# Optimization experiments

Hardware: AMD Instinct MI355X
Metric: run time of the kernel (lower is better)

## Reference

```python
import jax, jax.numpy as jnp
import numpy as np

EPS = 1e-8
ANGULAR_WEIGHT = 0.1
L2_REG = 1e-4


def gram_schmidt_batch(A):
    # A: (B, 3, 3); orthogonalize the COLUMNS
    u1 = A[:, :, 0]
    e1 = u1 / (jnp.linalg.norm(u1, axis=1, keepdims=True) + EPS)
    a2 = A[:, :, 1]
    u2 = a2 - jnp.sum(e1 * a2, axis=1, keepdims=True) * e1
    e2 = u2 / (jnp.linalg.norm(u2, axis=1, keepdims=True) + EPS)
    a3 = A[:, :, 2]
    u3 = a3 - jnp.sum(e1 * a3, axis=1, keepdims=True) * e1 - jnp.sum(e2 * a3, axis=1, keepdims=True) * e2
    e3 = u3 / (jnp.linalg.norm(u3, axis=1, keepdims=True) + EPS)
    Q = jnp.stack([e1, e2, e3], axis=2)  # (B,3,3), columns e1,e2,e3
    det = jnp.linalg.det(Q)
    # flip third column where det < 0 to ensure proper rotation
    e3_fixed = jnp.where(det[:, None] < 0, -Q[:, :, 2], Q[:, :, 2])
    return Q.at[:, :, 2].set(e3_fixed)


def nine_d_to_rotmat(nine_d):
    A = jnp.clip(nine_d, -10.0, 10.0).reshape(-1, 3, 3)
    return gram_schmidt_batch(A)


def angular_distance(pred_9d, target_9d):
    pred_rot = nine_d_to_rotmat(pred_9d)
    target_rot = nine_d_to_rotmat(target_9d)
    # trace(pred^T @ target) = sum over all entries of elementwise product
    traces = jnp.einsum('bij,bij->b', pred_rot, target_rot)
    traces = jnp.clip(traces, -3.0 + 1e-6, 3.0 - 1e-6)
    cos_angle = jnp.clip((traces - 1.0) / 2.0, -1.0 + 1e-7, 1.0 - 1e-7)
    angles_deg = jnp.arccos(cos_angle) * (180.0 / np.pi)
    return jnp.where(jnp.isnan(angles_deg), 180.0, angles_deg)


def orthogonality_loss(nine_d):
    B = nine_d.shape[0]
    M = nine_d.reshape(B, 3, 3)
    AtA = jnp.einsum('bki,bkj->bij', M, M)
    diff = AtA - jnp.eye(3, dtype=nine_d.dtype)
    return jnp.mean(jnp.sum(diff * diff, axis=(1, 2)))


def setup_inputs() -> dict:
    key = jax.random.key(0)
    k1, k2 = jax.random.split(key)
    B = 4194304
    return {
        'pred_delta_9d': jax.random.normal(k1, (B, 9), dtype=jnp.float32),
        'target_delta_9d': jax.random.normal(k2, (B, 9), dtype=jnp.float32),
    }


def reference(pred_delta_9d, target_delta_9d):
    pred_delta_9d = jnp.clip(pred_delta_9d, -10.0, 10.0)
    pred_rot = nine_d_to_rotmat(pred_delta_9d)
    target_rot = nine_d_to_rotmat(target_delta_9d)
    diff = pred_rot - target_rot
    chordal_loss = jnp.mean(jnp.sum(diff * diff, axis=(1, 2)))
    angular_loss_term = jnp.mean(angular_distance(pred_delta_9d, target_delta_9d))
    ortho_loss = orthogonality_loss(pred_delta_9d)
    l2_loss = jnp.mean(pred_delta_9d ** 2)
    total_loss = chordal_loss + ANGULAR_WEIGHT * angular_loss_term + 0.01 * ortho_loss + L2_REG * l2_loss
    # NaN fallback: MSE between pred and target
    fallback = jnp.mean((pred_delta_9d - target_delta_9d) ** 2)
    return jnp.where(jnp.isnan(total_loss), fallback, total_loss)
```

## Files before the change

kernel.cpp:

```cpp
#include <hip/hip_runtime.h>
#include <math.h>

#define EPS_GS 1e-8f
#define RAD2DEG 57.29577951308232f
#define PI_F 3.14159265358979f
#define NBLOCKS 2048
#define NTHREADS 256

__device__ __forceinline__ float clip10(float x) {
    x = x < -10.f ? -10.f : x;
    x = x >  10.f ?  10.f : x;
    return x;
}

__device__ __forceinline__ float fsqrt(float x) { return __builtin_amdgcn_sqrtf(x); }
__device__ __forceinline__ float frcp(float x)  { return __builtin_amdgcn_rcpf(x); }

__device__ __forceinline__ float fast_acos(float x) {
    float ax = fabsf(x);
    float p = fmaf(ax, -0.0187293f, 0.0742610f);
    p = fmaf(ax, p, -0.2121144f);
    p = fmaf(ax, p, 1.5707288f);
    float pos = fsqrt(1.f - ax) * p;
    return x >= 0.f ? pos : PI_F - pos;
}

__device__ __forceinline__ void gs_rotmat(const float* v, float* R) {
    float c0x = v[0], c0y = v[3], c0z = v[6];
    float c1x = v[1], c1y = v[4], c1z = v[7];
    float c2x = v[2], c2y = v[5], c2z = v[8];

    float s1 = fmaf(c0x, c0x, fmaf(c0y, c0y, c0z*c0z));
    float inv1 = frcp(fsqrt(s1) + EPS_GS);
    float e1x = c0x*inv1, e1y = c0y*inv1, e1z = c0z*inv1;

    float d = fmaf(e1x, c1x, fmaf(e1y, c1y, e1z*c1z));
    float u2x = fmaf(-d, e1x, c1x), u2y = fmaf(-d, e1y, c1y), u2z = fmaf(-d, e1z, c1z);
    float s2 = fmaf(u2x, u2x, fmaf(u2y, u2y, u2z*u2z));
    float inv2 = frcp(fsqrt(s2) + EPS_GS);
    float e2x = u2x*inv2, e2y = u2y*inv2, e2z = u2z*inv2;

    float d1 = fmaf(e1x, c2x, fmaf(e1y, c2y, e1z*c2z));
    float d2 = fmaf(e2x, c2x, fmaf(e2y, c2y, e2z*c2z));
    float u3x = fmaf(-d1, e1x, fmaf(-d2, e2x, c2x));
    float u3y = fmaf(-d1, e1y, fmaf(-d2, e2y, c2y));
    float u3z = fmaf(-d1, e1z, fmaf(-d2, e2z, c2z));
    float s3 = fmaf(u3x, u3x, fmaf(u3y, u3y, u3z*u3z));
    float inv3 = frcp(fsqrt(s3) + EPS_GS);
    float e3x = u3x*inv3, e3y = u3y*inv3, e3z = u3z*inv3;

    float cxx = e2y*e3z - e2z*e3y;
    float cxy = e2z*e3x - e2x*e3z;
    float cxz = e2x*e3y - e2y*e3x;
    float det = fmaf(e1x, cxx, fmaf(e1y, cxy, e1z*cxz));
    if (det < 0.f) { e3x = -e3x; e3y = -e3y; e3z = -e3z; }

    R[0] = e1x; R[1] = e2x; R[2] = e3x;
    R[3] = e1y; R[4] = e2y; R[5] = e3y;
    R[6] = e1z; R[7] = e2z; R[8] = e3z;
}

__device__ __forceinline__ void accum_rot(const float* pr, const float* tg,
                                          float& lt, float& lf) {
    float pc[9], tc[9];
    #pragma unroll
    for (int m = 0; m < 9; ++m) { pc[m] = clip10(pr[m]); tc[m] = clip10(tg[m]); }

    float Rp[9], Rt[9];
    gs_rotmat(pc, Rp);
    gs_rotmat(tc, Rt);

    float chord = 0.f, tr = 0.f;
    #pragma unroll
    for (int m = 0; m < 9; ++m) {
        float d = Rp[m] - Rt[m];
        chord = fmaf(d, d, chord);
        tr    = fmaf(Rp[m], Rt[m], tr);
    }

    const float trLo = -3.0f + 1e-6f, trHi = 3.0f - 1e-6f;
    tr = tr < trLo ? trLo : (tr > trHi ? trHi : tr);
    float ca = (tr - 1.f) * 0.5f;
    const float cLo = -1.0f + 1e-7f, cHi = 1.0f - 1e-7f;
    ca = ca < cLo ? cLo : (ca > cHi ? cHi : ca);
    float ang = fast_acos(ca) * RAD2DEG;
    if (ang != ang) ang = 180.f;

    float o = 0.f;
    #pragma unroll
    for (int i = 0; i < 3; ++i) {
        #pragma unroll
        for (int j = 0; j < 3; ++j) {
            float s = fmaf(pc[i], pc[j], fmaf(pc[3+i], pc[3+j], pc[6+i]*pc[6+j]));
            s -= (i == j) ? 1.f : 0.f;
            o = fmaf(s, s, o);
        }
    }

    float l2 = 0.f, fb = 0.f;
    #pragma unroll
    for (int m = 0; m < 9; ++m) {
        l2 = fmaf(pc[m], pc[m], l2);
        float d = pc[m] - tg[m];
        fb = fmaf(d, d, fb);
    }

    lt += fmaf(0.1f, ang, chord) + fmaf(0.01f, o, (1e-4f/9.f)*l2);
    lf += fb;
}

__global__ __launch_bounds__(NTHREADS)
void rot_loss_kernel(const float* __restrict__ pred, const float* __restrict__ targ,
                     float2* __restrict__ partial, int B) {
    const int ngroups  = (B + 3) >> 2;
    const int nthreads = gridDim.x * blockDim.x;

    float lt = 0.f, lf = 0.f;

    for (int g = blockIdx.x * blockDim.x + threadIdx.x; g < ngroups; g += nthreads) {
        const int base = g * 4;
        if (base + 3 < B) {
            const float4* p4 = reinterpret_cast<const float4*>(pred) + (size_t)g * 9;
            const float4* t4 = reinterpret_cast<const float4*>(targ) + (size_t)g * 9;
            float4 pv[9], tv[9];
            #pragma unroll
            for (int j = 0; j < 9; ++j) pv[j] = p4[j];
            #pragma unroll
            for (int j = 0; j < 9; ++j) tv[j] = t4[j];
            float a[36], b[36];
            #pragma unroll
            for (int j = 0; j < 9; ++j) {
                a[4*j+0] = pv[j].x; a[4*j+1] = pv[j].y; a[4*j+2] = pv[j].z; a[4*j+3] = pv[j].w;
                b[4*j+0] = tv[j].x; b[4*j+1] = tv[j].y; b[4*j+2] = tv[j].z; b[4*j+3] = tv[j].w;
            }
            #pragma unroll
            for (int k = 0; k < 4; ++k) accum_rot(&a[9*k], &b[9*k], lt, lf);
        } else {
            for (int r = base; r < B; ++r) {
                float a1[9], b1[9];
                for (int m = 0; m < 9; ++m) { a1[m] = pred[(size_t)r*9 + m]; b1[m] = targ[(size_t)r*9 + m]; }
                accum_rot(a1, b1, lt, lf);
            }
        }
    }

    #pragma unroll
    for (int off = 32; off > 0; off >>= 1) {
        lt += __shfl_down(lt, off, 64);
        lf += __shfl_down(lf, off, 64);
    }
    __shared__ float st[4], sf[4];
    const int lane = threadIdx.x & 63;
    const int wid  = threadIdx.x >> 6;
    if (lane == 0) { st[wid] = lt; sf[wid] = lf; }
    __syncthreads();
    if (threadIdx.x == 0) {
        float bt = st[0] + st[1] + st[2] + st[3];
        float bf = sf[0] + sf[1] + sf[2] + sf[3];
        partial[blockIdx.x] = make_float2(bt, bf);
    }
}

__global__ __launch_bounds__(256)
void finalize_kernel(const float2* __restrict__ partial, int nparts,
                     float* __restrict__ out, int B) {
    double t = 0.0, f = 0.0;
    for (int i = threadIdx.x; i < nparts; i += 256) {
        float2 p = partial[i];
        t += (double)p.x;
        f += (double)p.y;
    }
    #pragma unroll
    for (int off = 32; off > 0; off >>= 1) {
        t += __shfl_down(t, off, 64);
        f += __shfl_down(f, off, 64);
    }
    __shared__ double st[4], sf[4];
    const int lane = threadIdx.x & 63;
    const int wid  = threadIdx.x >> 6;
    if (lane == 0) { st[wid] = t; sf[wid] = f; }
    __syncthreads();
    if (threadIdx.x == 0) {
        double total = (st[0] + st[1] + st[2] + st[3]) / (double)B;
        double fb    = (sf[0] + sf[1] + sf[2] + sf[3]) / (9.0 * (double)B);
        out[0] = isnan(total) ? (float)fb : (float)total;
    }
}

extern "C" void kernel_launch(void* const* d_in, const int* in_sizes, int n_in,
                              void* d_out, int out_size, void* d_ws, size_t ws_size,
                              hipStream_t stream) {
    const float* pred = (const float*)d_in[0];
    const float* targ = (const float*)d_in[1];
    const int n = in_sizes[0];
    const int B = n / 9;

    float2* partial = (float2*)d_ws;

    rot_loss_kernel<<<NBLOCKS, NTHREADS, 0, stream>>>(pred, targ, partial, B);
    finalize_kernel<<<1, 256, 0, stream>>>(partial, NBLOCKS, (float*)d_out, B);
}
```

Before: 368.6 us.

## Stage rotations through shared memory with coalesced loads, one tile per block

Replaces the grid-stride loop, where each thread loaded 9 strided float4s, with a one-shot kernel. Each block loads 512 rotations of pred and target into LDS using fully coalesced float4 reads, then each thread computes two rotations from LDS. A separate tail kernel handles leftover rows, and the finalize kernel grows to 1024 threads to reduce the larger set of partials (8192 blocks). The cost is 36 KB of LDS per block, which limits occupancy, plus strided 9-float LDS reads per thread that may bank-conflict.

```diff
diff --git a/kernel.cpp b/kernel.cpp
--- a/kernel.cpp
+++ b/kernel.cpp
@@ -4,8 +4,8 @@
 #define EPS_GS 1e-8f
 #define RAD2DEG 57.29577951308232f
 #define PI_F 3.14159265358979f
-#define NBLOCKS 2048
-#define NTHREADS 256
+#define ROT_PER_BLOCK 512
+#define F4_PER_INPUT 1152
 
 __device__ __forceinline__ float clip10(float x) {
     x = x < -10.f ? -10.f : x;
@@ -109,41 +109,7 @@
     lf += fb;
 }
 
-__global__ __launch_bounds__(NTHREADS)
-void rot_loss_kernel(const float* __restrict__ pred, const float* __restrict__ targ,
-                     float2* __restrict__ partial, int B) {
-    const int ngroups  = (B + 3) >> 2;
-    const int nthreads = gridDim.x * blockDim.x;
-
-    float lt = 0.f, lf = 0.f;
-
-    for (int g = blockIdx.x * blockDim.x + threadIdx.x; g < ngroups; g += nthreads) {
-        const int base = g * 4;
-        if (base + 3 < B) {
-            const float4* p4 = reinterpret_cast<const float4*>(pred) + (size_t)g * 9;
-            const float4* t4 = reinterpret_cast<const float4*>(targ) + (size_t)g * 9;
-            float4 pv[9], tv[9];
-            #pragma unroll
-            for (int j = 0; j < 9; ++j) pv[j] = p4[j];
-            #pragma unroll
-            for (int j = 0; j < 9; ++j) tv[j] = t4[j];
-            float a[36], b[36];
-            #pragma unroll
-            for (int j = 0; j < 9; ++j) {
-                a[4*j+0] = pv[j].x; a[4*j+1] = pv[j].y; a[4*j+2] = pv[j].z; a[4*j+3] = pv[j].w;
-                b[4*j+0] = tv[j].x; b[4*j+1] = tv[j].y; b[4*j+2] = tv[j].z; b[4*j+3] = tv[j].w;
-            }
-            #pragma unroll
-            for (int k = 0; k < 4; ++k) accum_rot(&a[9*k], &b[9*k], lt, lf);
-        } else {
-            for (int r = base; r < B; ++r) {
-                float a1[9], b1[9];
-                for (int m = 0; m < 9; ++m) { a1[m] = pred[(size_t)r*9 + m]; b1[m] = targ[(size_t)r*9 + m]; }
-                accum_rot(a1, b1, lt, lf);
-            }
-        }
-    }
-
+__device__ __forceinline__ float2 block_reduce(float lt, float lf) {
     #pragma unroll
     for (int off = 32; off > 0; off >>= 1) {
         lt += __shfl_down(lt, off, 64);
@@ -154,18 +120,72 @@
     const int wid  = threadIdx.x >> 6;
     if (lane == 0) { st[wid] = lt; sf[wid] = lf; }
     __syncthreads();
+    float2 r = make_float2(0.f, 0.f);
     if (threadIdx.x == 0) {
-        float bt = st[0] + st[1] + st[2] + st[3];
-        float bf = sf[0] + sf[1] + sf[2] + sf[3];
-        partial[blockIdx.x] = make_float2(bt, bf);
-    }
+        int nw = (blockDim.x + 63) >> 6;
+        for (int w = 0; w < nw; ++w) { r.x += st[w]; r.y += sf[w]; }
+    }
+    return r;
 }
 
 __global__ __launch_bounds__(256)
+void rot_loss_kernel(const float* __restrict__ pred, const float* __restrict__ targ,
+                     float2* __restrict__ partial) {
+    __shared__ float sP[ROT_PER_BLOCK * 9];
+    __shared__ float sT[ROT_PER_BLOCK * 9];
+
+    const int tid = threadIdx.x;
+    const size_t base4 = (size_t)blockIdx.x * F4_PER_INPUT;
+    const float4* p4 = reinterpret_cast<const float4*>(pred) + base4;
+    const float4* t4 = reinterpret_cast<const float4*>(targ) + base4;
+    float4* sP4 = reinterpret_cast<float4*>(sP);
+    float4* sT4 = reinterpret_cast<float4*>(sT);
+
+    float4 rp[5], rt[5];
+    #pragma unroll
+    for (int j = 0; j < 5; ++j) {
+        int idx = tid + 256 * j;
+        if (idx < F4_PER_INPUT) rp[j] = p4[idx];
+    }
+    #pragma unroll
+    for (int j = 0; j < 5; ++j) {
+        int idx = tid + 256 * j;
+        if (idx < F4_PER_INPUT) rt[j] = t4[idx];
+    }
+    #pragma unroll
+    for (int j = 0; j < 5; ++j) {
+        int idx = tid + 256 * j;
+        if (idx < F4_PER_INPUT) { sP4[idx] = rp[j]; sT4[idx] = rt[j]; }
+    }
+    __syncthreads();
+
+    float lt = 0.f, lf = 0.f;
+    accum_rot(&sP[tid * 9],         &sT[tid * 9],         lt, lf);
+    accum_rot(&sP[(tid + 256) * 9], &sT[(tid + 256) * 9], lt, lf);
+
+    float2 r = block_reduce(lt, lf);
+    if (threadIdx.x == 0) partial[blockIdx.x] = r;
+}
+
+__global__ __launch_bounds__(256)
+void rot_loss_tail(const float* __restrict__ pred, const float* __restrict__ targ,
+                   float2* __restrict__ partial, int pslot, int start, int B) {
+    int r = start + blockIdx.x * blockDim.x + threadIdx.x;
+    float lt = 0.f, lf = 0.f;
+    if (r < B) {
+        float a[9], b[9];
+        for (int m = 0; m < 9; ++m) { a[m] = pred[(size_t)r*9 + m]; b[m] = targ[(size_t)r*9 + m]; }
+        accum_rot(a, b, lt, lf);
+    }
+    float2 rr = block_reduce(lt, lf);
+    if (threadIdx.x == 0) partial[pslot + blockIdx.x] = rr;
+}
+
+__global__ __launch_bounds__(1024)
 void finalize_kernel(const float2* __restrict__ partial, int nparts,
                      float* __restrict__ out, int B) {
     double t = 0.0, f = 0.0;
-    for (int i = threadIdx.x; i < nparts; i += 256) {
+    for (int i = threadIdx.x; i < nparts; i += 1024) {
         float2 p = partial[i];
         t += (double)p.x;
         f += (double)p.y;
@@ -175,14 +195,16 @@
         t += __shfl_down(t, off, 64);
         f += __shfl_down(f, off, 64);
     }
-    __shared__ double st[4], sf[4];
+    __shared__ double st[16], sf[16];
     const int lane = threadIdx.x & 63;
     const int wid  = threadIdx.x >> 6;
     if (lane == 0) { st[wid] = t; sf[wid] = f; }
     __syncthreads();
     if (threadIdx.x == 0) {
-        double total = (st[0] + st[1] + st[2] + st[3]) / (double)B;
-        double fb    = (sf[0] + sf[1] + sf[2] + sf[3]) / (9.0 * (double)B);
+        double tt = 0.0, ff = 0.0;
+        for (int w = 0; w < 16; ++w) { tt += st[w]; ff += sf[w]; }
+        double total = tt / (double)B;
+        double fb    = ff / (9.0 * (double)B);
         out[0] = isnan(total) ? (float)fb : (float)total;
     }
 }
@@ -197,6 +219,14 @@
 
     float2* partial = (float2*)d_ws;
 
-    rot_loss_kernel<<<NBLOCKS, NTHREADS, 0, stream>>>(pred, targ, partial, B);
-    finalize_kernel<<<1, 256, 0, stream>>>(partial, NBLOCKS, (float*)d_out, B);
-}
+    const int fullBlocks = B / ROT_PER_BLOCK;
+    const int rem        = B - fullBlocks * ROT_PER_BLOCK;
+    const int tailBlocks = (rem + 255) / 256;
+    if (fullBlocks > 0)
+        rot_loss_kernel<<<fullBlocks, 256, 0, stream>>>(pred, targ, partial);
+    if (rem > 0)
+        rot_loss_tail<<<tailBlocks, 256, 0, stream>>>(
+            pred, targ, partial, fullBlocks, fullBlocks * ROT_PER_BLOCK, B);
+    finalize_kernel<<<1, 1024, 0, stream>>>(partial, fullBlocks + tailBlocks,
+                                            (float*)d_out, B);
+}
```

New measurement: 370.5 us. No clear change (+0.5%).
